# Optimization experiments

Hardware: AMD Instinct MI355X
Metric: run time of the kernel (lower is better)

The kernel has to match this reference:

```python
import jax, jax.numpy as jnp
import numpy as np
from math import sqrt

B, S, H, NH = 4, 1024, 1024, 16
HS = H // NH
ALPHA = 2.0


def apply_rope(x, dis):
    # x: [B,S,NH,HS], dis: [B,S,1,HS] = [sin || cos]
    dis_sin, dis_cos = jnp.split(dis, 2, axis=-1)
    x0, x1 = x[..., 0::2], x[..., 1::2]
    return jnp.concatenate([x0 * dis_cos - x1 * dis_sin,
                            x1 * dis_cos + x0 * dis_sin], axis=-1)


def setup_inputs() -> dict:
    key = jax.random.key(0)
    ks = jax.random.split(key, 12)
    tgt = jax.random.normal(ks[0], (B, S, H), dtype=jnp.float32)
    # causal mask so every softmax row has at least one valid key
    tgt_mask = jnp.tril(jnp.ones((S, S), dtype=bool))[None, None]  # [1,1,S,S]
    tgt_mask = jnp.broadcast_to(tgt_mask, (B, 1, S, S))
    glycan_mass = jax.random.uniform(ks[1], (B, S, 1, HS), dtype=jnp.float32)
    glycan_query_mass = jax.random.uniform(ks[2], (B, S, 1, HS), dtype=jnp.float32)
    s = 1.0 / np.sqrt(H)
    Wq = jax.random.normal(ks[3], (H, H), dtype=jnp.float32) * s
    Wk = jax.random.normal(ks[4], (H, H), dtype=jnp.float32) * s
    Wv = jax.random.normal(ks[5], (H, H), dtype=jnp.float32) * (0.5 * s)  # beta gain
    Wo = jax.random.normal(ks[6], (H, H), dtype=jnp.float32) * (0.5 * s)
    bq = jnp.zeros((H,), jnp.float32)
    bk = jnp.zeros((H,), jnp.float32)
    bv = jnp.zeros((H,), jnp.float32)
    bo = jnp.zeros((H,), jnp.float32)
    ln_w = jnp.ones((H,), jnp.float32)
    ln_b = jnp.zeros((H,), jnp.float32)
    return {"tgt": tgt, "tgt_mask": tgt_mask, "glycan_mass": glycan_mass,
            "glycan_query_mass": glycan_query_mass,
            "Wq": Wq, "bq": bq, "Wk": Wk, "bk": bk, "Wv": Wv, "bv": bv,
            "Wo": Wo, "bo": bo, "ln_w": ln_w, "ln_b": ln_b}


def reference(tgt, tgt_mask, glycan_mass, glycan_query_mass,
              Wq, bq, Wk, bk, Wv, bv, Wo, bo, ln_w, ln_b):
    b = tgt.shape[0]
    q = (tgt @ Wq + bq).reshape(b, -1, NH, HS)
    k = (tgt @ Wk + bk).reshape(b, -1, NH, HS)
    v = (tgt @ Wv + bv).reshape(b, -1, NH, HS)
    q = apply_rope(q, glycan_query_mass)
    k = apply_rope(k, glycan_mass)
    # attn: [b, head, q_pos, k_pos]
    attn = jnp.einsum('bnij,bmij->binm', q, k) / sqrt(HS)
    attn = jnp.where(tgt_mask, attn, -jnp.inf)
    attn = jax.nn.softmax(attn, axis=-1)
    postx = jnp.einsum('binm,bmij->bnij', attn, v).reshape(b, -1, H)
    postx = postx @ Wo + bo
    # DeepNorm (dropout = identity at inference)
    x = tgt * ALPHA + postx
    mu = jnp.mean(x, axis=-1, keepdims=True)
    var = jnp.var(x, axis=-1, keepdims=True)
    return (x - mu) / jnp.sqrt(var + 1e-5) * ln_w + ln_b
```

## Files before the change

### kernel.cpp

```cpp
#include <hip/hip_runtime.h>

#define NB 4
#define NS 1024
#define NHID 1024
#define NHEAD 16
#define HDIM 64

typedef unsigned short u16;
typedef __bf16 bf16x8 __attribute__((ext_vector_type(8)));
typedef float f32x4 __attribute__((ext_vector_type(4)));
typedef u16 us8 __attribute__((ext_vector_type(8)));
typedef u16 us4 __attribute__((ext_vector_type(4)));

__device__ __forceinline__ u16 f2b(float f) {
  union { float f; unsigned u; } v; v.f = f;
  unsigned r = v.u + 0x7fffu + ((v.u >> 16) & 1u);
  return (u16)(r >> 16);
}
__device__ __forceinline__ float b2f(u16 b) {
  union { unsigned u; float f; } v; v.u = ((unsigned)b) << 16;
  return v.f;
}
__device__ __forceinline__ bf16x8 as_bf(us8 v) {
  bf16x8 r; __builtin_memcpy(&r, &v, sizeof(r)); return r;
}

__global__ void k_wt(const float* __restrict__ Wq, const float* __restrict__ Wk,
                     const float* __restrict__ Wv, const float* __restrict__ Wo,
                     u16* __restrict__ out) {
  const float* W = (blockIdx.z == 0) ? Wq : (blockIdx.z == 1) ? Wk
                   : (blockIdx.z == 2) ? Wv : Wo;
  u16* o = out + (size_t)blockIdx.z * NHID * NHID;
  __shared__ u16 tl[64][65];
  const int n0 = blockIdx.x * 64, k0 = blockIdx.y * 64;
  const int tr = threadIdx.x >> 4, tc = (threadIdx.x & 15) * 4;
#pragma unroll
  for (int rr = tr; rr < 64; rr += 16) {
    float4 v = *(const float4*)(W + (size_t)(k0 + rr) * NHID + n0 + tc);
    tl[rr][tc + 0] = f2b(v.x);
    tl[rr][tc + 1] = f2b(v.y);
    tl[rr][tc + 2] = f2b(v.z);
    tl[rr][tc + 3] = f2b(v.w);
  }
  __syncthreads();
#pragma unroll
  for (int rr = tr; rr < 64; rr += 16) {
    us4 v;
    v[0] = tl[tc + 0][rr];
    v[1] = tl[tc + 1][rr];
    v[2] = tl[tc + 2][rr];
    v[3] = tl[tc + 3][rr];
    *(us4*)(o + (size_t)(n0 + rr) * NHID + k0 + tc) = v;
  }
}

__global__ __launch_bounds__(256, 2) void k_gemm_qkv(
    const float* __restrict__ tgt, const u16* __restrict__ Wt,
    const float* __restrict__ bq, const float* __restrict__ bk,
    const float* __restrict__ bv, u16* __restrict__ Qb, u16* __restrict__ Kb,
    u16* __restrict__ Vb) {
  const int z = blockIdx.z;
  const u16* Wz = Wt + (size_t)z * NHID * NHID;
  const float* bias = (z == 0) ? bq : (z == 1) ? bk : bv;
  u16* outp = (z == 0) ? Qb : (z == 1) ? Kb : Vb;

  __shared__ u16 As[128 * 64];
  __shared__ u16 Bs[128 * 64];

  const int t = threadIdx.x;
  const int m0 = blockIdx.y * 128, n0 = blockIdx.x * 128;
  const int w = t >> 6, lane = t & 63, lq = lane & 15, lk = lane >> 4;
  const int wm = (w >> 1) * 64, wn = (w & 1) * 64;

  f32x4 acc[4][4];
#pragma unroll
  for (int i = 0; i < 4; i++)
#pragma unroll
    for (int j = 0; j < 4; j++) acc[i][j] = (f32x4){0.f, 0.f, 0.f, 0.f};

  for (int k0 = 0; k0 < NHID; k0 += 64) {
    __syncthreads();
#pragma unroll
    for (int i = 0; i < 4; i++) {
      int idx = t + i * 256;
      int r = idx >> 3, ch = idx & 7;
      const float* ap = tgt + (size_t)(m0 + r) * NHID + k0 + ch * 8;
      float4 a0 = *(const float4*)ap;
      float4 a1 = *(const float4*)(ap + 4);
      us8 va;
      va[0] = f2b(a0.x); va[1] = f2b(a0.y); va[2] = f2b(a0.z); va[3] = f2b(a0.w);
      va[4] = f2b(a1.x); va[5] = f2b(a1.y); va[6] = f2b(a1.z); va[7] = f2b(a1.w);
      *(us8*)(As + r * 64 + ((ch ^ (r & 7)) << 3)) = va;
      us8 vb = *(const us8*)(Wz + (size_t)(n0 + r) * NHID + k0 + ch * 8);
      *(us8*)(Bs + r * 64 + ((ch ^ (r & 7)) << 3)) = vb;
    }
    __syncthreads();
#pragma unroll
    for (int kk = 0; kk < 2; kk++) {
      bf16x8 af[4], bfv[4];
#pragma unroll
      for (int m = 0; m < 4; m++) {
        int r = wm + m * 16 + lq;
        int ch = kk * 4 + lk;
        af[m] = as_bf(*(const us8*)(As + r * 64 + ((ch ^ (r & 7)) << 3)));
      }
#pragma unroll
      for (int n = 0; n < 4; n++) {
        int r = wn + n * 16 + lq;
        int ch = kk * 4 + lk;
        bfv[n] = as_bf(*(const us8*)(Bs + r * 64 + ((ch ^ (r & 7)) << 3)));
      }
#pragma unroll
      for (int m = 0; m < 4; m++)
#pragma unroll
        for (int n = 0; n < 4; n++)
          acc[m][n] = __builtin_amdgcn_mfma_f32_16x16x32_bf16(af[m], bfv[n],
                                                              acc[m][n], 0, 0, 0);
    }
  }
#pragma unroll
  for (int m = 0; m < 4; m++)
#pragma unroll
    for (int n = 0; n < 4; n++) {
      int gn = n0 + wn + n * 16 + lq;
      int h = gn >> 6, d = gn & 63;
      float bval = bias[gn];
#pragma unroll
      for (int r = 0; r < 4; r++) {
        int gm = m0 + wm + m * 16 + 4 * lk + r;
        int b = gm >> 10, s = gm & 1023;
        float v = acc[m][n][r] + bval;
        outp[(((size_t)(b * NHEAD + h) * NS + s) << 6) + d] = f2b(v);
      }
    }
}

__global__ void k_rope(u16* __restrict__ Qb, u16* __restrict__ Kb,
                       const float* __restrict__ qmass,
                       const float* __restrict__ kmass) {
  int id = blockIdx.x * 256 + threadIdx.x;
  int which = id >> 16;
  int r = id & 65535;
  int s = r & 1023;
  int b = r >> 14;
  u16* ptr = (which ? Kb : Qb) + ((size_t)r << 6);
  const float* dis = (which ? kmass : qmass) + ((size_t)(b * NS + s) << 6);
  float x[64];
#pragma unroll
  for (int c8 = 0; c8 < 8; c8++) {
    us8 v = *(const us8*)(ptr + c8 * 8);
#pragma unroll
    for (int j = 0; j < 8; j++) x[c8 * 8 + j] = b2f(v[j]);
  }
  us8 outv[8];
#pragma unroll
  for (int c = 0; c < 32; c++) {
    float sn = dis[c], cs = dis[32 + c];
    float x0 = x[2 * c], x1 = x[2 * c + 1];
    outv[c >> 3][c & 7] = f2b(x0 * cs - x1 * sn);
    outv[(c >> 3) + 4][c & 7] = f2b(x1 * cs + x0 * sn);
  }
#pragma unroll
  for (int c8 = 0; c8 < 8; c8++) *(us8*)(ptr + c8 * 8) = outv[c8];
}

__global__ __launch_bounds__(256, 2) void k_attn(const u16* __restrict__ Qb,
                                                 const u16* __restrict__ Kb,
                                                 const u16* __restrict__ Vb,
                                                 u16* __restrict__ Ob) {
  const int qt = (int)gridDim.x - 1 - (int)blockIdx.x;
  const int h = blockIdx.y, b = blockIdx.z;
  const size_t hoff = ((size_t)(b * NHEAD + h)) * NS * HDIM;
  const u16* Qh = Qb + hoff;
  const u16* Kh = Kb + hoff;
  const u16* Vh = Vb + hoff;

  __shared__ u16 Ks[64 * 64];
  __shared__ u16 Vs[64 * 64];
  __shared__ u16 Ps[4][1024];

  const int t = threadIdx.x, w = t >> 6, lane = t & 63;
  const int lq = lane & 15, lk = lane >> 4;

  bf16x8 qf[2];
  {
    const u16* qr = Qh + (size_t)(qt * 64 + w * 16 + lq) * 64;
    qf[0] = as_bf(*(const us8*)(qr + lk * 8));
    qf[1] = as_bf(*(const us8*)(qr + 32 + lk * 8));
  }

  f32x4 oacc[4];
#pragma unroll
  for (int i = 0; i < 4; i++) oacc[i] = (f32x4){0.f, 0.f, 0.f, 0.f};
  float mrun[4] = {-1e30f, -1e30f, -1e30f, -1e30f};
  float lrun[4] = {0.f, 0.f, 0.f, 0.f};

  for (int kt = 0; kt <= qt; ++kt) {
    __syncthreads();
#pragma unroll
    for (int i = 0; i < 2; i++) {
      int idx = t + i * 256;
      int s = idx >> 3, ch = idx & 7;
      us8 kv = *(const us8*)(Kh + (size_t)(kt * 64 + s) * 64 + ch * 8);
      *(us8*)(Ks + s * 64 + ((ch ^ (s & 7)) << 3)) = kv;
      us8 vv = *(const us8*)(Vh + (size_t)(kt * 64 + s) * 64 + ch * 8);
#pragma unroll
      for (int j = 0; j < 8; j++) {
        int d = ch * 8 + j;
        Vs[d * 64 + (((s >> 3) ^ (d & 7)) << 3) + (s & 7)] = vv[j];
      }
    }
    __syncthreads();

    f32x4 sfr[4];
#pragma unroll
    for (int fc = 0; fc < 4; fc++) {
      f32x4 a = (f32x4){0.f, 0.f, 0.f, 0.f};
#pragma unroll
      for (int kk = 0; kk < 2; kk++) {
        int r = fc * 16 + lq;
        int ch = kk * 4 + lk;
        bf16x8 kf = as_bf(*(const us8*)(Ks + r * 64 + ((ch ^ (r & 7)) << 3)));
        a = __builtin_amdgcn_mfma_f32_16x16x32_bf16(qf[kk], kf, a, 0, 0, 0);
      }
      sfr[fc] = a;
    }
    const float sc = 0.125f;
    if (kt == qt) {
#pragma unroll
      for (int fc = 0; fc < 4; fc++)
#pragma unroll
        for (int r = 0; r < 4; r++) {
          int qrow = w * 16 + 4 * lk + r;
          int kcol = fc * 16 + lq;
          sfr[fc][r] = (kcol <= qrow) ? sfr[fc][r] * sc : -1e30f;
        }
    } else {
#pragma unroll
      for (int fc = 0; fc < 4; fc++)
#pragma unroll
        for (int r = 0; r < 4; r++) sfr[fc][r] *= sc;
    }
    float pv[4][4];
#pragma unroll
    for (int r = 0; r < 4; r++) {
      float mx = fmaxf(fmaxf(sfr[0][r], sfr[1][r]), fmaxf(sfr[2][r], sfr[3][r]));
#pragma unroll
      for (int d = 1; d < 16; d <<= 1) mx = fmaxf(mx, __shfl_xor(mx, d));
      float mn = fmaxf(mrun[r], mx);
      float corr = __expf(mrun[r] - mn);
      float rs = 0.f;
#pragma unroll
      for (int fc = 0; fc < 4; fc++) {
        float p = __expf(sfr[fc][r] - mn);
        pv[fc][r] = p;
        rs += p;
      }
#pragma unroll
      for (int d = 1; d < 16; d <<= 1) rs += __shfl_xor(rs, d);
      mrun[r] = mn;
      lrun[r] = lrun[r] * corr + rs;
#pragma unroll
      for (int fc = 0; fc < 4; fc++) oacc[fc][r] *= corr;
    }
    u16* Pw = Ps[w];
#pragma unroll
    for (int fc = 0; fc < 4; fc++)
#pragma unroll
      for (int r = 0; r < 4; r++) {
        int i = 4 * lk + r, c = fc * 16 + lq;
        Pw[i * 64 + (((c >> 3) ^ (i & 7)) << 3) + (c & 7)] = f2b(pv[fc][r]);
      }
    bf16x8 pf[2];
#pragma unroll
    for (int kk = 0; kk < 2; kk++) {
      int ch = kk * 4 + lk;
      pf[kk] = as_bf(*(const us8*)(Pw + lq * 64 + ((ch ^ (lq & 7)) << 3)));
    }
#pragma unroll
    for (int fc = 0; fc < 4; fc++)
#pragma unroll
      for (int kk = 0; kk < 2; kk++) {
        int r = fc * 16 + lq;
        int ch = kk * 4 + lk;
        bf16x8 vf = as_bf(*(const us8*)(Vs + r * 64 + ((ch ^ (r & 7)) << 3)));
        oacc[fc] = __builtin_amdgcn_mfma_f32_16x16x32_bf16(pf[kk], vf, oacc[fc],
                                                           0, 0, 0);
      }
  }
#pragma unroll
  for (int fc = 0; fc < 4; fc++)
#pragma unroll
    for (int r = 0; r < 4; r++) {
      int qrow = qt * 64 + w * 16 + 4 * lk + r;
      float o = oacc[fc][r] / lrun[r];
      Ob[((size_t)(b * NS + qrow) << 10) + h * 64 + fc * 16 + lq] = f2b(o);
    }
}

__global__ __launch_bounds__(256, 2) void k_gemm_o(
    const u16* __restrict__ Ab, const u16* __restrict__ Wz,
    const float* __restrict__ bo, const float* __restrict__ tgt,
    u16* __restrict__ xb) {
  __shared__ u16 As[128 * 64];
  __shared__ u16 Bs[128 * 64];

  const int t = threadIdx.x;
  const int m0 = blockIdx.y * 128, n0 = blockIdx.x * 128;
  const int w = t >> 6, lane = t & 63, lq = lane & 15, lk = lane >> 4;
  const int wm = (w >> 1) * 64, wn = (w & 1) * 64;

  f32x4 acc[4][4];
#pragma unroll
  for (int i = 0; i < 4; i++)
#pragma unroll
    for (int j = 0; j < 4; j++) acc[i][j] = (f32x4){0.f, 0.f, 0.f, 0.f};

  for (int k0 = 0; k0 < NHID; k0 += 64) {
    __syncthreads();
#pragma unroll
    for (int i = 0; i < 4; i++) {
      int idx = t + i * 256;
      int r = idx >> 3, ch = idx & 7;
      us8 va = *(const us8*)(Ab + (size_t)(m0 + r) * NHID + k0 + ch * 8);
      *(us8*)(As + r * 64 + ((ch ^ (r & 7)) << 3)) = va;
      us8 vb = *(const us8*)(Wz + (size_t)(n0 + r) * NHID + k0 + ch * 8);
      *(us8*)(Bs + r * 64 + ((ch ^ (r & 7)) << 3)) = vb;
    }
    __syncthreads();
#pragma unroll
    for (int kk = 0; kk < 2; kk++) {
      bf16x8 af[4], bfv[4];
#pragma unroll
      for (int m = 0; m < 4; m++) {
        int r = wm + m * 16 + lq;
        int ch = kk * 4 + lk;
        af[m] = as_bf(*(const us8*)(As + r * 64 + ((ch ^ (r & 7)) << 3)));
      }
#pragma unroll
      for (int n = 0; n < 4; n++) {
        int r = wn + n * 16 + lq;
        int ch = kk * 4 + lk;
        bfv[n] = as_bf(*(const us8*)(Bs + r * 64 + ((ch ^ (r & 7)) << 3)));
      }
#pragma unroll
      for (int m = 0; m < 4; m++)
#pragma unroll
        for (int n = 0; n < 4; n++)
          acc[m][n] = __builtin_amdgcn_mfma_f32_16x16x32_bf16(af[m], bfv[n],
                                                              acc[m][n], 0, 0, 0);
    }
  }
#pragma unroll
  for (int m = 0; m < 4; m++)
#pragma unroll
    for (int n = 0; n < 4; n++) {
      int gn = n0 + wn + n * 16 + lq;
      float bval = bo[gn];
#pragma unroll
      for (int r = 0; r < 4; r++) {
        int gm = m0 + wm + m * 16 + 4 * lk + r;
        float v = acc[m][n][r] + bval + 2.0f * tgt[((size_t)gm << 10) + gn];
        xb[((size_t)gm << 10) + gn] = f2b(v);
      }
    }
}

__global__ void k_ln(const u16* __restrict__ xb, const float* __restrict__ lw,
                     const float* __restrict__ lb, float* __restrict__ out) {
  const int row = blockIdx.x, t = threadIdx.x;
  const u16* xr = xb + ((size_t)row << 10);
  us4 v = *(const us4*)(xr + t * 4);
  float f[4];
  float s = 0.f, sq = 0.f;
#pragma unroll
  for (int j = 0; j < 4; j++) {
    f[j] = b2f(v[j]);
    s += f[j];
    sq += f[j] * f[j];
  }
#pragma unroll
  for (int d = 1; d < 64; d <<= 1) {
    s += __shfl_xor(s, d);
    sq += __shfl_xor(sq, d);
  }
  __shared__ float ss[4], sk[4];
  int w = t >> 6, lane = t & 63;
  if (lane == 0) {
    ss[w] = s;
    sk[w] = sq;
  }
  __syncthreads();
  s = ss[0] + ss[1] + ss[2] + ss[3];
  sq = sk[0] + sk[1] + sk[2] + sk[3];
  float mean = s * (1.0f / 1024.0f);
  float var = sq * (1.0f / 1024.0f) - mean * mean;
  float rstd = rsqrtf(var + 1e-5f);
  float4 o;
#pragma unroll
  for (int j = 0; j < 4; j++) {
    int c = t * 4 + j;
    ((float*)&o)[j] = (f[j] - mean) * rstd * lw[c] + lb[c];
  }
  *(float4*)(out + ((size_t)row << 10) + t * 4) = o;
}

extern "C" void kernel_launch(void* const* d_in, const int* in_sizes, int n_in,
                              void* d_out, int out_size, void* d_ws,
                              size_t ws_size, hipStream_t stream) {
  const float* tgt = (const float*)d_in[0];
  const float* kmass = (const float*)d_in[2];
  const float* qmass = (const float*)d_in[3];
  const float* Wq = (const float*)d_in[4];
  const float* bq = (const float*)d_in[5];
  const float* Wk = (const float*)d_in[6];
  const float* bk = (const float*)d_in[7];
  const float* Wv = (const float*)d_in[8];
  const float* bv = (const float*)d_in[9];
  const float* Wo = (const float*)d_in[10];
  const float* bo = (const float*)d_in[11];
  const float* lw = (const float*)d_in[12];
  const float* lb = (const float*)d_in[13];
  float* out = (float*)d_out;

  char* ws = (char*)d_ws;
  u16* Wt = (u16*)ws;
  u16* Qb = (u16*)(ws + (8u << 20));
  u16* Kb = (u16*)(ws + (16u << 20));
  u16* Vb = (u16*)(ws + (24u << 20));
  u16* Ob = (u16*)(ws + (32u << 20));
  u16* xb = (u16*)(ws + (8u << 20));

  k_wt<<<dim3(16, 16, 4), 256, 0, stream>>>(Wq, Wk, Wv, Wo, Wt);
  k_gemm_qkv<<<dim3(8, 32, 3), 256, 0, stream>>>(tgt, Wt, bq, bk, bv, Qb, Kb, Vb);
  k_rope<<<512, 256, 0, stream>>>(Qb, Kb, qmass, kmass);
  k_attn<<<dim3(16, NHEAD, NB), 256, 0, stream>>>(Qb, Kb, Vb, Ob);
  k_gemm_o<<<dim3(8, 32), 256, 0, stream>>>(Ob, Wt + 3u * NHID * NHID, bo, tgt, xb);
  k_ln<<<4096, 256, 0, stream>>>(xb, lw, lb, out);
}
```

Measured before the change: 279.4 us.

## Emit V transposed from QKV GEMM and load attention K/V fragments directly

After: 304.5 us. 9.0% more time.

```diff
diff --git a/kernel.cpp b/kernel.cpp
--- a/kernel.cpp
+++ b/kernel.cpp
@@ -58,17 +58,18 @@
     const float* __restrict__ tgt, const u16* __restrict__ Wt,
     const float* __restrict__ bq, const float* __restrict__ bk,
     const float* __restrict__ bv, u16* __restrict__ Qb, u16* __restrict__ Kb,
-    u16* __restrict__ Vb) {
+    u16* __restrict__ VTb) {
   const int z = blockIdx.z;
   const u16* Wz = Wt + (size_t)z * NHID * NHID;
   const float* bias = (z == 0) ? bq : (z == 1) ? bk : bv;
-  u16* outp = (z == 0) ? Qb : (z == 1) ? Kb : Vb;
+  const bool vt = (z == 2);
+  const int m0 = (vt ? blockIdx.x : blockIdx.y) * 128;
+  const int n0 = (vt ? blockIdx.y : blockIdx.x) * 128;
 
   __shared__ u16 As[128 * 64];
   __shared__ u16 Bs[128 * 64];
 
   const int t = threadIdx.x;
-  const int m0 = blockIdx.y * 128, n0 = blockIdx.x * 128;
   const int w = t >> 6, lane = t & 63, lq = lane & 15, lk = lane >> 4;
   const int wm = (w >> 1) * 64, wn = (w & 1) * 64;
 
@@ -84,14 +85,23 @@
     for (int i = 0; i < 4; i++) {
       int idx = t + i * 256;
       int r = idx >> 3, ch = idx & 7;
-      const float* ap = tgt + (size_t)(m0 + r) * NHID + k0 + ch * 8;
-      float4 a0 = *(const float4*)ap;
-      float4 a1 = *(const float4*)(ap + 4);
-      us8 va;
-      va[0] = f2b(a0.x); va[1] = f2b(a0.y); va[2] = f2b(a0.z); va[3] = f2b(a0.w);
-      va[4] = f2b(a1.x); va[5] = f2b(a1.y); va[6] = f2b(a1.z); va[7] = f2b(a1.w);
+      us8 va, vb;
+      if (!vt) {
+        const float* ap = tgt + (size_t)(m0 + r) * NHID + k0 + ch * 8;
+        float4 a0 = *(const float4*)ap;
+        float4 a1 = *(const float4*)(ap + 4);
+        va[0] = f2b(a0.x); va[1] = f2b(a0.y); va[2] = f2b(a0.z); va[3] = f2b(a0.w);
+        va[4] = f2b(a1.x); va[5] = f2b(a1.y); va[6] = f2b(a1.z); va[7] = f2b(a1.w);
+        vb = *(const us8*)(Wz + (size_t)(n0 + r) * NHID + k0 + ch * 8);
+      } else {
+        va = *(const us8*)(Wz + (size_t)(m0 + r) * NHID + k0 + ch * 8);
+        const float* bp = tgt + (size_t)(n0 + r) * NHID + k0 + ch * 8;
+        float4 b0 = *(const float4*)bp;
+        float4 b1 = *(const float4*)(bp + 4);
+        vb[0] = f2b(b0.x); vb[1] = f2b(b0.y); vb[2] = f2b(b0.z); vb[3] = f2b(b0.w);
+        vb[4] = f2b(b1.x); vb[5] = f2b(b1.y); vb[6] = f2b(b1.z); vb[7] = f2b(b1.w);
+      }
       *(us8*)(As + r * 64 + ((ch ^ (r & 7)) << 3)) = va;
-      us8 vb = *(const us8*)(Wz + (size_t)(n0 + r) * NHID + k0 + ch * 8);
       *(us8*)(Bs + r * 64 + ((ch ^ (r & 7)) << 3)) = vb;
     }
     __syncthreads();
@@ -118,21 +128,39 @@
                                                               acc[m][n], 0, 0, 0);
     }
   }
-#pragma unroll
-  for (int m = 0; m < 4; m++)
-#pragma unroll
-    for (int n = 0; n < 4; n++) {
-      int gn = n0 + wn + n * 16 + lq;
-      int h = gn >> 6, d = gn & 63;
-      float bval = bias[gn];
-#pragma unroll
-      for (int r = 0; r < 4; r++) {
-        int gm = m0 + wm + m * 16 + 4 * lk + r;
-        int b = gm >> 10, s = gm & 1023;
-        float v = acc[m][n][r] + bval;
-        outp[(((size_t)(b * NHEAD + h) * NS + s) << 6) + d] = f2b(v);
-      }
-    }
+  if (!vt) {
+#pragma unroll
+    for (int m = 0; m < 4; m++)
+#pragma unroll
+      for (int n = 0; n < 4; n++) {
+        int gn = n0 + wn + n * 16 + lq;
+        int h = gn >> 6, d = gn & 63;
+        float bval = bias[gn];
+#pragma unroll
+        for (int r = 0; r < 4; r++) {
+          int gm = m0 + wm + m * 16 + 4 * lk + r;
+          int b = gm >> 10, s = gm & 1023;
+          float v = acc[m][n][r] + bval;
+          ((z == 0) ? Qb : Kb)[(((size_t)(b * NHEAD + h) * NS + s) << 6) + d] =
+              f2b(v);
+        }
+      }
+  } else {
+#pragma unroll
+    for (int m = 0; m < 4; m++)
+#pragma unroll
+      for (int n = 0; n < 4; n++) {
+        int gn = n0 + wn + n * 16 + lq;
+        int b = gn >> 10, s = gn & 1023;
+#pragma unroll
+        for (int r = 0; r < 4; r++) {
+          int gm = m0 + wm + m * 16 + 4 * lk + r;
+          int h = gm >> 6, d = gm & 63;
+          float v = acc[m][n][r] + bias[gm];
+          VTb[(((size_t)(b * NHEAD + h)) << 16) + ((size_t)d << 10) + s] = f2b(v);
+        }
+      }
+  }
 }
 
 __global__ void k_rope(u16* __restrict__ Qb, u16* __restrict__ Kb,
@@ -166,17 +194,18 @@
 
 __global__ __launch_bounds__(256, 2) void k_attn(const u16* __restrict__ Qb,
                                                  const u16* __restrict__ Kb,
-                                                 const u16* __restrict__ Vb,
+                                                 const u16* __restrict__ VTb,
                                                  u16* __restrict__ Ob) {
-  const int qt = (int)gridDim.x - 1 - (int)blockIdx.x;
-  const int h = blockIdx.y, b = blockIdx.z;
-  const size_t hoff = ((size_t)(b * NHEAD + h)) * NS * HDIM;
+  const int id = blockIdx.x;
+  const int wrk = (id & 7) * 128 + (id >> 3);
+  const int bh = wrk >> 4;
+  const int qt = 15 - (wrk & 15);
+  const int b = bh >> 4, h = bh & 15;
+  const size_t hoff = (size_t)bh << 16;
   const u16* Qh = Qb + hoff;
   const u16* Kh = Kb + hoff;
-  const u16* Vh = Vb + hoff;
-
-  __shared__ u16 Ks[64 * 64];
-  __shared__ u16 Vs[64 * 64];
+  const u16* VTh = VTb + hoff;
+
   __shared__ u16 Ps[4][1024];
 
   const int t = threadIdx.x, w = t >> 6, lane = t & 63;
@@ -196,33 +225,30 @@
   float lrun[4] = {0.f, 0.f, 0.f, 0.f};
 
   for (int kt = 0; kt <= qt; ++kt) {
-    __syncthreads();
-#pragma unroll
-    for (int i = 0; i < 2; i++) {
-      int idx = t + i * 256;
-      int s = idx >> 3, ch = idx & 7;
-      us8 kv = *(const us8*)(Kh + (size_t)(kt * 64 + s) * 64 + ch * 8);
-      *(us8*)(Ks + s * 64 + ((ch ^ (s & 7)) << 3)) = kv;
-      us8 vv = *(const us8*)(Vh + (size_t)(kt * 64 + s) * 64 + ch * 8);
-#pragma unroll
-      for (int j = 0; j < 8; j++) {
-        int d = ch * 8 + j;
-        Vs[d * 64 + (((s >> 3) ^ (d & 7)) << 3) + (s & 7)] = vv[j];
-      }
-    }
-    __syncthreads();
+    const u16* kb = Kh + ((size_t)kt << 12);
+    us8 kfr[4][2];
+#pragma unroll
+    for (int fc = 0; fc < 4; fc++)
+#pragma unroll
+      for (int kk = 0; kk < 2; kk++)
+        kfr[fc][kk] =
+            *(const us8*)(kb + (fc * 16 + lq) * 64 + (kk * 4 + lk) * 8);
+    us8 vfr[4][2];
+#pragma unroll
+    for (int fc = 0; fc < 4; fc++)
+#pragma unroll
+      for (int kk = 0; kk < 2; kk++)
+        vfr[fc][kk] = *(const us8*)(VTh + ((size_t)(fc * 16 + lq) << 10) +
+                                    kt * 64 + (kk * 4 + lk) * 8);
 
     f32x4 sfr[4];
 #pragma unroll
     for (int fc = 0; fc < 4; fc++) {
       f32x4 a = (f32x4){0.f, 0.f, 0.f, 0.f};
 #pragma unroll
-      for (int kk = 0; kk < 2; kk++) {
-        int r = fc * 16 + lq;
-        int ch = kk * 4 + lk;
-        bf16x8 kf = as_bf(*(const us8*)(Ks + r * 64 + ((ch ^ (r & 7)) << 3)));
-        a = __builtin_amdgcn_mfma_f32_16x16x32_bf16(qf[kk], kf, a, 0, 0, 0);
-      }
+      for (int kk = 0; kk < 2; kk++)
+        a = __builtin_amdgcn_mfma_f32_16x16x32_bf16(qf[kk], as_bf(kfr[fc][kk]),
+                                                    a, 0, 0, 0);
       sfr[fc] = a;
     }
     const float sc = 0.125f;
@@ -280,13 +306,9 @@
 #pragma unroll
     for (int fc = 0; fc < 4; fc++)
 #pragma unroll
-      for (int kk = 0; kk < 2; kk++) {
-        int r = fc * 16 + lq;
-        int ch = kk * 4 + lk;
-        bf16x8 vf = as_bf(*(const us8*)(Vs + r * 64 + ((ch ^ (r & 7)) << 3)));
-        oacc[fc] = __builtin_amdgcn_mfma_f32_16x16x32_bf16(pf[kk], vf, oacc[fc],
-                                                           0, 0, 0);
-      }
+      for (int kk = 0; kk < 2; kk++)
+        oacc[fc] = __builtin_amdgcn_mfma_f32_16x16x32_bf16(
+            pf[kk], as_bf(vfr[fc][kk]), oacc[fc], 0, 0, 0);
   }
 #pragma unroll
   for (int fc = 0; fc < 4; fc++)
@@ -427,14 +449,16 @@
   u16* Wt = (u16*)ws;
   u16* Qb = (u16*)(ws + (8u << 20));
   u16* Kb = (u16*)(ws + (16u << 20));
-  u16* Vb = (u16*)(ws + (24u << 20));
+  u16* VTb = (u16*)(ws + (24u << 20));
   u16* Ob = (u16*)(ws + (32u << 20));
   u16* xb = (u16*)(ws + (8u << 20));
 
   k_wt<<<dim3(16, 16, 4), 256, 0, stream>>>(Wq, Wk, Wv, Wo, Wt);
-  k_gemm_qkv<<<dim3(8, 32, 3), 256, 0, stream>>>(tgt, Wt, bq, bk, bv, Qb, Kb, Vb);
+  k_gemm_qkv<<<dim3(8, 32, 3), 256, 0, stream>>>(tgt, Wt, bq, bk, bv, Qb, Kb,
+                                                 VTb);
   k_rope<<<512, 256, 0, stream>>>(Qb, Kb, qmass, kmass);
-  k_attn<<<dim3(16, NHEAD, NB), 256, 0, stream>>>(Qb, Kb, Vb, Ob);
-  k_gemm_o<<<dim3(8, 32), 256, 0, stream>>>(Ob, Wt + 3u * NHID * NHID, bo, tgt, xb);
+  k_attn<<<1024, 256, 0, stream>>>(Qb, Kb, VTb, Ob);
+  k_gemm_o<<<dim3(8, 32), 256, 0, stream>>>(Ob, Wt + 3u * NHID * NHID, bo, tgt,
+                                            xb);
   k_ln<<<4096, 256, 0, stream>>>(xb, lw, lb, out);
 }
```
